# Kernel optimization log

Measured on AMD Instinct MI355X. Metric: run time of the kernel, lower is better.

The kernel has to match this reference:

```python
import jax, jax.numpy as jnp
import numpy as np

D_EMB = 64
N_HEADS = 8
D_K = D_EMB // N_HEADS


def setup_inputs() -> dict:
    key = jax.random.key(0)
    ks = jax.random.split(key, 7)
    B, N = 4, 512
    s = 0.02
    return {
        "n": jax.random.normal(ks[0], (B, N, D_EMB), jnp.float32),
        "e": jax.random.normal(ks[1], (B, N, N, D_EMB), jnp.float32),
        # weights stored as (in, out); torch Linear applies x @ W.T
        "W_qkv": jax.random.normal(ks[2], (D_EMB, 3 * D_EMB), jnp.float32) * s,
        "O_n": jax.random.normal(ks[3], (D_EMB, D_EMB), jnp.float32) * s,
        "W_g": jax.random.normal(ks[4], (D_EMB, N_HEADS), jnp.float32) * s,
        "W_e": jax.random.normal(ks[5], (D_EMB, N_HEADS), jnp.float32) * s,
        "O_e": jax.random.normal(ks[6], (N_HEADS, D_EMB), jnp.float32) * s,
    }


def reference(n, e, W_qkv, O_n, W_g, W_e, O_e):
    B, N, _ = n.shape
    H, dk = N_HEADS, D_K
    # QKV projection -> [B, H, N, dk] each
    qkv = (n @ W_qkv).reshape(B, N, 3, H, dk)
    Q = jnp.transpose(qkv[:, :, 0], (0, 2, 1, 3))
    K = jnp.transpose(qkv[:, :, 1], (0, 2, 1, 3))
    V = jnp.transpose(qkv[:, :, 2], (0, 2, 1, 3))
    # per-head edge bias E and gate G: [B, H, N, N]
    E = jnp.transpose(e @ W_e, (0, 3, 1, 2))
    G = jax.nn.sigmoid(jnp.transpose(e @ W_g, (0, 3, 1, 2)))
    dynamic_centrality = jnp.log1p(G.sum(-1))  # [B, H, N]
    # scaled, clamped attention scores plus edge bias
    A_raw = jnp.einsum("bhnd,bhmd->bhnm", Q, K) * (dk ** -0.5)
    A_raw = jnp.clip(A_raw, -5.0, 5.0)
    _E = A_raw + E  # pre-softmax scores, reused for edge output
    A = jax.nn.softmax(_E, axis=-1)
    _V = jnp.einsum("bhnm,bhmd->bhnd", A, V)
    _V = _V * dynamic_centrality[..., None]  # centrality rescale
    n_out = jnp.transpose(_V, (0, 2, 1, 3)).reshape(B, N, H * dk) @ O_n
    e_out = jnp.transpose(_E, (0, 2, 3, 1)) @ O_e  # [B, N, N, d_emb]
    return (n_out, e_out)
```

## Files before the change

### kernel.cpp

```cpp
#include <hip/hip_runtime.h>

#define NN 512
#define SCALE 0.35355339059327373f
#define SMAX 6.0f

typedef short bf16x8 __attribute__((ext_vector_type(8)));
typedef float f32x4 __attribute__((ext_vector_type(4)));

__device__ __forceinline__ unsigned short bhi16(float x) {
    return (unsigned short)(__float_as_uint(x) >> 16);
}
__device__ __forceinline__ float btrunc(float x) {
    return __uint_as_float(__float_as_uint(x) & 0xFFFF0000u);
}
__device__ __forceinline__ unsigned short blo16(float x) {
    return (unsigned short)(__float_as_uint(x - btrunc(x)) >> 16);
}

__global__ __launch_bounds__(64) void qkv_proj(const float* __restrict__ nin,
                                               const float* __restrict__ Wqkv,
                                               float* __restrict__ qkv) {
    const int r = blockIdx.x;
    const int j = threadIdx.x;
    const float* nr = nin + (size_t)r * 64;
    float a0 = 0.f, a1 = 0.f, a2 = 0.f;
#pragma unroll
    for (int d = 0; d < 64; ++d) {
        const float nv = nr[d];
        const float* wr = Wqkv + d * 192;
        a0 = fmaf(nv, wr[j], a0);
        a1 = fmaf(nv, wr[64 + j], a1);
        a2 = fmaf(nv, wr[128 + j], a2);
    }
    float* o = qkv + (size_t)r * 192;
    o[j] = a0; o[64 + j] = a1; o[128 + j] = a2;
}

__device__ __forceinline__ void gload16(const float* g, float* l) {
    __builtin_amdgcn_global_load_lds(
        (const __attribute__((address_space(1))) unsigned int*)(g),
        (__attribute__((address_space(3))) unsigned int*)(l), 16, 0, 0);
}
#define WAITV(N) asm volatile("s_waitcnt vmcnt(" #N ")" ::: "memory")
#define BARRIER() __builtin_amdgcn_s_barrier()
#define SBAR() __builtin_amdgcn_sched_barrier(0)

__global__ __launch_bounds__(256, 3) void edge_mfma3(
    const float* __restrict__ e,
    const float* __restrict__ qkv,
    const float* __restrict__ We,
    const float* __restrict__ Wg,
    const float* __restrict__ Oe,
    const float* __restrict__ On,
    float* __restrict__ n_out,
    float* __restrict__ e_out)
{
    __shared__ float ebuf[4][2][16][64];
    __shared__ float E_lds[4][128][8];
    __shared__ float red[256];
    __shared__ float wdn[4][8], wgs[4][8];
    __shared__ float vfin[64];

    const int t = threadIdx.x, w = t >> 6, l = t & 63;
    const int a2 = l >> 4;
    const int m16 = l & 15;
    const int bid = blockIdx.x;
    const int bn = (bid & 7) * 256 + (bid >> 3);
    const int b = bn >> 9;
    const int rowbase = w * 128;
    const float* __restrict__ Q = qkv + (size_t)bn * 192;
    const float* __restrict__ ebase = e + (size_t)bn * 32768;
    float* __restrict__ eob = e_out + (size_t)bn * 32768;

    bf16x8 WfB[4], WcB[2], QdB[2];
#pragma unroll
    for (int blk = 0; blk < 4; ++blk) {
#pragma unroll
        for (int jj = 0; jj < 4; ++jj) {
            const int d = blk * 16 + a2 * 4 + jj;
            const float wv = (m16 < 8) ? We[d * 8 + m16] : Wg[d * 8 + m16 - 8];
            const short h = (short)bhi16(wv);
            WfB[blk][2 * jj] = h;
            WfB[blk][2 * jj + 1] = h;
        }
    }
#pragma unroll
    for (int c = 0; c < 2; ++c) {
        const int head = c * 4 + a2;
#pragma unroll
        for (int j = 0; j < 8; ++j) {
            const int d = c * 32 + a2 * 8 + j;
            const float wv = (m16 < 8) ? We[d * 8 + m16] : Wg[d * 8 + m16 - 8];
            WcB[c][j] = (short)blo16(wv);
            QdB[c][j] = (m16 == head) ? (short)bhi16(Q[d]) : (short)0;
        }
    }
    float dn = 0.f, gs = 0.f;
    SBAR();

#define STAGE(s) do {                                                            \
        _Pragma("unroll")                                                        \
        for (int i_ = 0; i_ < 4; ++i_) {                                         \
            const int lrow_ = i_ * 4 + (l >> 4);                                 \
            gload16(ebase + (size_t)(rowbase + (s) * 16 + lrow_) * 64            \
                        + (((l & 15) ^ lrow_) * 4),                              \
                    &ebuf[w][(s) & 1][i_ * 4][0]);                               \
        } } while (0)

#define SLAB(s, WN) do {                                                         \
        float4 kq0, kq1, kq2, kq3;                                               \
        { const float* kp_ = qkv + (size_t)(b * NN + rowbase + (s) * 16 + m16) * 192 \
                             + 64 + a2 * 8;                                      \
          kq0 = *(const float4*)(kp_);      kq1 = *(const float4*)(kp_ + 4);     \
          kq2 = *(const float4*)(kp_ + 32); kq3 = *(const float4*)(kp_ + 36); }  \
        SBAR();                                                                  \
        if ((s) < 7) STAGE((s) + 1);                                             \
        SBAR(); BARRIER(); WAITV(WN); SBAR();                                    \
        f32x4 c1 = {0.f, 0.f, 0.f, 0.f}, c2 = {0.f, 0.f, 0.f, 0.f};             \
        _Pragma("unroll")                                                        \
        for (int blk = 0; blk < 4; ++blk) {                                      \
            const float4 ev = *(const float4*)&ebuf[w][(s) & 1][m16]             \
                                  [(((blk * 4 + a2) ^ m16) * 4)];                \
            bf16x8 af;                                                           \
            af[0] = (short)bhi16(ev.x); af[1] = (short)blo16(ev.x);              \
            af[2] = (short)bhi16(ev.y); af[3] = (short)blo16(ev.y);              \
            af[4] = (short)bhi16(ev.z); af[5] = (short)blo16(ev.z);              \
            af[6] = (short)bhi16(ev.w); af[7] = (short)blo16(ev.w);              \
            c1 = __builtin_amdgcn_mfma_f32_16x16x32_bf16(af, WfB[blk], c1, 0, 0, 0); \
        }                                                                        \
        _Pragma("unroll")                                                        \
        for (int c = 0; c < 2; ++c) {                                            \
            const int g0 = c * 8 + a2 * 2;                                       \
            const float4 e0 = *(const float4*)&ebuf[w][(s) & 1][m16][((g0 ^ m16) * 4)]; \
            const float4 e1 = *(const float4*)&ebuf[w][(s) & 1][m16][(((g0 + 1) ^ m16) * 4)]; \
            bf16x8 ac;                                                           \
            ac[0] = (short)bhi16(e0.x); ac[1] = (short)bhi16(e0.y);              \
            ac[2] = (short)bhi16(e0.z); ac[3] = (short)bhi16(e0.w);              \
            ac[4] = (short)bhi16(e1.x); ac[5] = (short)bhi16(e1.y);              \
            ac[6] = (short)bhi16(e1.z); ac[7] = (short)bhi16(e1.w);              \
            c1 = __builtin_amdgcn_mfma_f32_16x16x32_bf16(ac, WcB[c], c1, 0, 0, 0); \
            const float4 k0 = (c == 0) ? kq0 : kq2;                              \
            const float4 k1 = (c == 0) ? kq1 : kq3;                              \
            bf16x8 kf;                                                           \
            kf[0] = (short)bhi16(k0.x); kf[1] = (short)bhi16(k0.y);              \
            kf[2] = (short)bhi16(k0.z); kf[3] = (short)bhi16(k0.w);              \
            kf[4] = (short)bhi16(k1.x); kf[5] = (short)bhi16(k1.y);              \
            kf[6] = (short)bhi16(k1.z); kf[7] = (short)bhi16(k1.w);              \
            c2 = __builtin_amdgcn_mfma_f32_16x16x32_bf16(kf, QdB[c], c2, 0, 0, 0); \
        }                                                                        \
        if (m16 < 8) {                                                           \
            _Pragma("unroll")                                                    \
            for (int r = 0; r < 4; ++r) {                                        \
                const float E_ = fminf(fmaxf(c2[r] * SCALE, -5.f), 5.f) + c1[r]; \
                dn += __expf(E_ - SMAX);                                         \
                E_lds[w][(s) * 16 + a2 * 4 + r][m16] = E_;                       \
            }                                                                    \
        } else {                                                                 \
            _Pragma("unroll")                                                    \
            for (int r = 0; r < 4; ++r) gs += 1.f / (1.f + __expf(-c1[r]));      \
        } } while (0)

    STAGE(0);
    SLAB(0, 8); SLAB(1, 8); SLAB(2, 8); SLAB(3, 8);
    SLAB(4, 8); SLAB(5, 8); SLAB(6, 8); SLAB(7, 0);

    {
        const int j4 = l & 15, mr = l >> 4;
        float oc[8][4];
#pragma unroll
        for (int h = 0; h < 8; ++h) {
            const float4 v = reinterpret_cast<const float4*>(Oe + h * 64 + j4 * 4)[0];
            oc[h][0] = v.x; oc[h][1] = v.y; oc[h][2] = v.z; oc[h][3] = v.w;
        }
#pragma unroll 4
        for (int p = 0; p < 32; ++p) {
            const int mloc = p * 4 + mr;
            const float* er = &E_lds[w][mloc][0];
            const float4 ra = *reinterpret_cast<const float4*>(er);
            const float4 rb = *reinterpret_cast<const float4*>(er + 4);
            float o0 = ra.x * oc[0][0], o1 = ra.x * oc[0][1], o2 = ra.x * oc[0][2], o3 = ra.x * oc[0][3];
            o0 = fmaf(ra.y, oc[1][0], o0); o1 = fmaf(ra.y, oc[1][1], o1); o2 = fmaf(ra.y, oc[1][2], o2); o3 = fmaf(ra.y, oc[1][3], o3);
            o0 = fmaf(ra.z, oc[2][0], o0); o1 = fmaf(ra.z, oc[2][1], o1); o2 = fmaf(ra.z, oc[2][2], o2); o3 = fmaf(ra.z, oc[2][3], o3);
            o0 = fmaf(ra.w, oc[3][0], o0); o1 = fmaf(ra.w, oc[3][1], o1); o2 = fmaf(ra.w, oc[3][2], o2); o3 = fmaf(ra.w, oc[3][3], o3);
            o0 = fmaf(rb.x, oc[4][0], o0); o1 = fmaf(rb.x, oc[4][1], o1); o2 = fmaf(rb.x, oc[4][2], o2); o3 = fmaf(rb.x, oc[4][3], o3);
            o0 = fmaf(rb.y, oc[5][0], o0); o1 = fmaf(rb.y, oc[5][1], o1); o2 = fmaf(rb.y, oc[5][2], o2); o3 = fmaf(rb.y, oc[5][3], o3);
            o0 = fmaf(rb.z, oc[6][0], o0); o1 = fmaf(rb.z, oc[6][1], o1); o2 = fmaf(rb.z, oc[6][2], o2); o3 = fmaf(rb.z, oc[6][3], o3);
            o0 = fmaf(rb.w, oc[7][0], o0); o1 = fmaf(rb.w, oc[7][1], o1); o2 = fmaf(rb.w, oc[7][2], o2); o3 = fmaf(rb.w, oc[7][3], o3);
            reinterpret_cast<float4*>(eob + (size_t)(rowbase + mloc) * 64 + j4 * 4)[0]
                = make_float4(o0, o1, o2, o3);
        }
    }

    dn += __shfl_xor(dn, 16, 64); dn += __shfl_xor(dn, 32, 64);
    gs += __shfl_xor(gs, 16, 64); gs += __shfl_xor(gs, 32, 64);
    if (a2 == 0 && m16 < 8) wdn[w][m16] = dn;
    if (a2 == 0 && m16 >= 8) wgs[w][m16 - 8] = gs;

    {
        const int k = l & 7, hh = (l >> 3) & 7;
        const float* vb = qkv + (size_t)(b * NN + rowbase) * 192 + 128 + hh * 8 + k;
        float acc = 0.f;
#pragma unroll 8
        for (int i = 0; i < 128; ++i) {
            const float p = __expf(E_lds[w][i][hh] - SMAX);
            acc = fmaf(p, vb[(size_t)i * 192], acc);
        }
        red[t] = acc;
    }
    __syncthreads();
    if (t < 64) {
        const int hh = t >> 3;
        const float den = wdn[0][hh] + wdn[1][hh] + wdn[2][hh] + wdn[3][hh];
        const float gsum = wgs[0][hh] + wgs[1][hh] + wgs[2][hh] + wgs[3][hh];
        vfin[t] = (red[t] + red[64 + t] + red[128 + t] + red[192 + t]) * (1.f / den) * log1pf(gsum);
    }
    __syncthreads();
    {
        float acc = 0.f;
#pragma unroll
        for (int i = w * 16; i < w * 16 + 16; ++i)
            acc = fmaf(vfin[i], On[i * 64 + l], acc);
        red[t] = acc;
    }
    __syncthreads();
    if (t < 64)
        n_out[(size_t)bn * 64 + t] = red[t] + red[64 + t] + red[128 + t] + red[192 + t];

#undef STAGE
#undef SLAB
}

extern "C" void kernel_launch(void* const* d_in, const int* in_sizes, int n_in,
                              void* d_out, int out_size, void* d_ws, size_t ws_size,
                              hipStream_t stream) {
    const float* n_in_p = (const float*)d_in[0];
    const float* e_p    = (const float*)d_in[1];
    const float* Wqkv   = (const float*)d_in[2];
    const float* On     = (const float*)d_in[3];
    const float* Wg     = (const float*)d_in[4];
    const float* We     = (const float*)d_in[5];
    const float* Oe     = (const float*)d_in[6];
    float* out = (float*)d_out;
    float* n_out = out;
    float* e_out = out + (size_t)4 * 512 * 64;
    float* qkv = (float*)d_ws;

    hipLaunchKernelGGL(qkv_proj, dim3(4 * NN), dim3(64), 0, stream, n_in_p, Wqkv, qkv);
    hipLaunchKernelGGL(edge_mfma3, dim3(4 * NN), dim3(256), 0, stream,
                       e_p, qkv, We, Wg, Oe, On, n_out, e_out);
}
```

Baseline: 188.6 us.

## Split each query row across four workgroups and finalize node output in separate kernel

The edge kernel now handles a quarter of the key rows per workgroup (32 rows per wave instead of 128), launching 8192 blocks with occupancy hint raised to 4. Partial softmax numerators, denominators and gate sums are written to workspace, and a new small kernel combines them and applies the centrality scale and O_n projection. Scheduling barriers and the inter-wave barrier in the slab pipeline are removed, and the pipeline depth per wave shrinks to two slabs. This aims for more parallelism and latency hiding, at the cost of an extra launch, workspace traffic and repeated per-block weight setup.

```diff
diff --git a/kernel.cpp b/kernel.cpp
--- a/kernel.cpp
+++ b/kernel.cpp
@@ -42,32 +42,30 @@
         (__attribute__((address_space(3))) unsigned int*)(l), 16, 0, 0);
 }
 #define WAITV(N) asm volatile("s_waitcnt vmcnt(" #N ")" ::: "memory")
-#define BARRIER() __builtin_amdgcn_s_barrier()
-#define SBAR() __builtin_amdgcn_sched_barrier(0)
-
-__global__ __launch_bounds__(256, 3) void edge_mfma3(
+
+__global__ __launch_bounds__(256, 4) void edge_mfma4(
     const float* __restrict__ e,
     const float* __restrict__ qkv,
     const float* __restrict__ We,
     const float* __restrict__ Wg,
     const float* __restrict__ Oe,
-    const float* __restrict__ On,
-    float* __restrict__ n_out,
-    float* __restrict__ e_out)
+    float* __restrict__ e_out,
+    float* __restrict__ pvw,
+    float* __restrict__ dngs)
 {
     __shared__ float ebuf[4][2][16][64];
-    __shared__ float E_lds[4][128][8];
+    __shared__ float E_lds[4][32][8];
     __shared__ float red[256];
     __shared__ float wdn[4][8], wgs[4][8];
-    __shared__ float vfin[64];
 
     const int t = threadIdx.x, w = t >> 6, l = t & 63;
     const int a2 = l >> 4;
     const int m16 = l & 15;
     const int bid = blockIdx.x;
-    const int bn = (bid & 7) * 256 + (bid >> 3);
+    const int wg = (bid & 7) * 1024 + (bid >> 3);
+    const int bn = wg >> 2, chunk = wg & 3;
     const int b = bn >> 9;
-    const int rowbase = w * 128;
+    const int rowc = chunk * 128 + w * 32;
     const float* __restrict__ Q = qkv + (size_t)bn * 192;
     const float* __restrict__ ebase = e + (size_t)bn * 32768;
     float* __restrict__ eob = e_out + (size_t)bn * 32768;
@@ -96,26 +94,24 @@
         }
     }
     float dn = 0.f, gs = 0.f;
-    SBAR();
 
 #define STAGE(s) do {                                                            \
         _Pragma("unroll")                                                        \
         for (int i_ = 0; i_ < 4; ++i_) {                                         \
             const int lrow_ = i_ * 4 + (l >> 4);                                 \
-            gload16(ebase + (size_t)(rowbase + (s) * 16 + lrow_) * 64            \
+            gload16(ebase + (size_t)(rowc + (s) * 16 + lrow_) * 64               \
                         + (((l & 15) ^ lrow_) * 4),                              \
                     &ebuf[w][(s) & 1][i_ * 4][0]);                               \
         } } while (0)
 
-#define SLAB(s, WN) do {                                                         \
+#define SLAB(s, PREF, WN) do {                                                   \
         float4 kq0, kq1, kq2, kq3;                                               \
-        { const float* kp_ = qkv + (size_t)(b * NN + rowbase + (s) * 16 + m16) * 192 \
+        { const float* kp_ = qkv + (size_t)(b * NN + rowc + (s) * 16 + m16) * 192 \
                              + 64 + a2 * 8;                                      \
           kq0 = *(const float4*)(kp_);      kq1 = *(const float4*)(kp_ + 4);     \
           kq2 = *(const float4*)(kp_ + 32); kq3 = *(const float4*)(kp_ + 36); }  \
-        SBAR();                                                                  \
-        if ((s) < 7) STAGE((s) + 1);                                             \
-        SBAR(); BARRIER(); WAITV(WN); SBAR();                                    \
+        if (PREF) STAGE((s) + 1);                                                \
+        WAITV(WN);                                                               \
         f32x4 c1 = {0.f, 0.f, 0.f, 0.f}, c2 = {0.f, 0.f, 0.f, 0.f};             \
         _Pragma("unroll")                                                        \
         for (int blk = 0; blk < 4; ++blk) {                                      \
@@ -161,8 +157,32 @@
         } } while (0)
 
     STAGE(0);
-    SLAB(0, 8); SLAB(1, 8); SLAB(2, 8); SLAB(3, 8);
-    SLAB(4, 8); SLAB(5, 8); SLAB(6, 8); SLAB(7, 0);
+    SLAB(0, 1, 4);
+    SLAB(1, 0, 4);
+
+    dn += __shfl_xor(dn, 16, 64); dn += __shfl_xor(dn, 32, 64);
+    gs += __shfl_xor(gs, 16, 64); gs += __shfl_xor(gs, 32, 64);
+    if (a2 == 0 && m16 < 8) wdn[w][m16] = dn;
+    if (a2 == 0 && m16 >= 8) wgs[w][m16 - 8] = gs;
+
+    {
+        const int k = l & 7, hh = (l >> 3) & 7;
+        const float* vb = qkv + (size_t)(b * NN + rowc) * 192 + 128 + hh * 8 + k;
+        float acc = 0.f;
+#pragma unroll 8
+        for (int i = 0; i < 32; ++i) {
+            const float p = __expf(E_lds[w][i][hh] - SMAX);
+            acc = fmaf(p, vb[(size_t)i * 192], acc);
+        }
+        red[t] = acc;
+    }
+    __syncthreads();
+    if (t < 64)
+        pvw[(size_t)wg * 64 + t] = red[t] + red[64 + t] + red[128 + t] + red[192 + t];
+    if (t < 8)
+        dngs[(size_t)wg * 16 + t] = wdn[0][t] + wdn[1][t] + wdn[2][t] + wdn[3][t];
+    else if (t < 16)
+        dngs[(size_t)wg * 16 + t] = wgs[0][t - 8] + wgs[1][t - 8] + wgs[2][t - 8] + wgs[3][t - 8];
 
     {
         const int j4 = l & 15, mr = l >> 4;
@@ -172,8 +192,8 @@
             const float4 v = reinterpret_cast<const float4*>(Oe + h * 64 + j4 * 4)[0];
             oc[h][0] = v.x; oc[h][1] = v.y; oc[h][2] = v.z; oc[h][3] = v.w;
         }
-#pragma unroll 4
-        for (int p = 0; p < 32; ++p) {
+#pragma unroll 2
+        for (int p = 0; p < 8; ++p) {
             const int mloc = p * 4 + mr;
             const float* er = &E_lds[w][mloc][0];
             const float4 ra = *reinterpret_cast<const float4*>(er);
@@ -186,48 +206,38 @@
             o0 = fmaf(rb.y, oc[5][0], o0); o1 = fmaf(rb.y, oc[5][1], o1); o2 = fmaf(rb.y, oc[5][2], o2); o3 = fmaf(rb.y, oc[5][3], o3);
             o0 = fmaf(rb.z, oc[6][0], o0); o1 = fmaf(rb.z, oc[6][1], o1); o2 = fmaf(rb.z, oc[6][2], o2); o3 = fmaf(rb.z, oc[6][3], o3);
             o0 = fmaf(rb.w, oc[7][0], o0); o1 = fmaf(rb.w, oc[7][1], o1); o2 = fmaf(rb.w, oc[7][2], o2); o3 = fmaf(rb.w, oc[7][3], o3);
-            reinterpret_cast<float4*>(eob + (size_t)(rowbase + mloc) * 64 + j4 * 4)[0]
+            reinterpret_cast<float4*>(eob + (size_t)(rowc + mloc) * 64 + j4 * 4)[0]
                 = make_float4(o0, o1, o2, o3);
         }
     }
-
-    dn += __shfl_xor(dn, 16, 64); dn += __shfl_xor(dn, 32, 64);
-    gs += __shfl_xor(gs, 16, 64); gs += __shfl_xor(gs, 32, 64);
-    if (a2 == 0 && m16 < 8) wdn[w][m16] = dn;
-    if (a2 == 0 && m16 >= 8) wgs[w][m16 - 8] = gs;
-
-    {
-        const int k = l & 7, hh = (l >> 3) & 7;
-        const float* vb = qkv + (size_t)(b * NN + rowbase) * 192 + 128 + hh * 8 + k;
-        float acc = 0.f;
-#pragma unroll 8
-        for (int i = 0; i < 128; ++i) {
-            const float p = __expf(E_lds[w][i][hh] - SMAX);
-            acc = fmaf(p, vb[(size_t)i * 192], acc);
-        }
-        red[t] = acc;
-    }
-    __syncthreads();
-    if (t < 64) {
-        const int hh = t >> 3;
-        const float den = wdn[0][hh] + wdn[1][hh] + wdn[2][hh] + wdn[3][hh];
-        const float gsum = wgs[0][hh] + wgs[1][hh] + wgs[2][hh] + wgs[3][hh];
-        vfin[t] = (red[t] + red[64 + t] + red[128 + t] + red[192 + t]) * (1.f / den) * log1pf(gsum);
-    }
-    __syncthreads();
-    {
-        float acc = 0.f;
-#pragma unroll
-        for (int i = w * 16; i < w * 16 + 16; ++i)
-            acc = fmaf(vfin[i], On[i * 64 + l], acc);
-        red[t] = acc;
-    }
-    __syncthreads();
-    if (t < 64)
-        n_out[(size_t)bn * 64 + t] = red[t] + red[64 + t] + red[128 + t] + red[192 + t];
-
 #undef STAGE
 #undef SLAB
+}
+
+__global__ __launch_bounds__(64) void nout_fin(
+    const float* __restrict__ pvw,
+    const float* __restrict__ dngs,
+    const float* __restrict__ On,
+    float* __restrict__ n_out)
+{
+    __shared__ float vfin[64];
+    const int bn = blockIdx.x, t = threadIdx.x;
+    const int hh = t >> 3;
+    float pv = 0.f, den = 0.f, gsum = 0.f;
+#pragma unroll
+    for (int c = 0; c < 4; ++c) {
+        const size_t wg = (size_t)bn * 4 + c;
+        pv += pvw[wg * 64 + t];
+        den += dngs[wg * 16 + hh];
+        gsum += dngs[wg * 16 + 8 + hh];
+    }
+    vfin[t] = pv * (1.f / den) * log1pf(gsum);
+    __syncthreads();
+    float acc = 0.f;
+#pragma unroll
+    for (int i = 0; i < 64; ++i)
+        acc = fmaf(vfin[i], On[i * 64 + t], acc);
+    n_out[(size_t)bn * 64 + t] = acc;
 }
 
 extern "C" void kernel_launch(void* const* d_in, const int* in_sizes, int n_in,
@@ -244,8 +254,12 @@
     float* n_out = out;
     float* e_out = out + (size_t)4 * 512 * 64;
     float* qkv = (float*)d_ws;
+    float* pvw = qkv + 393216;
+    float* dngs = pvw + 524288;
 
     hipLaunchKernelGGL(qkv_proj, dim3(4 * NN), dim3(64), 0, stream, n_in_p, Wqkv, qkv);
-    hipLaunchKernelGGL(edge_mfma3, dim3(4 * NN), dim3(256), 0, stream,
-                       e_p, qkv, We, Wg, Oe, On, n_out, e_out);
-}
+    hipLaunchKernelGGL(edge_mfma4, dim3(8192), dim3(256), 0, stream,
+                       e_p, qkv, We, Wg, Oe, e_out, pvw, dngs);
+    hipLaunchKernelGGL(nout_fin, dim3(4 * NN), dim3(64), 0, stream,
+                       pvw, dngs, On, n_out);
+}
```

Result: slower. 193.2 us (+2.4%).
